# Kernel optimization log

Measured on AMD Instinct MI355X. Metric: run time of the kernel, lower is better.

The kernel has to match this reference:

```python
import jax, jax.numpy as jnp
import numpy as np
from functools import partial

EPS = 1e-3  # keras LayerNormalization default epsilon

def _conv_same(inp, w):
    # inp: [B,H,W,Cin], w: [k,k,Cin,Cout]
    return jax.lax.conv_general_dilated(
        inp, w, window_strides=(1, 1), padding='SAME',
        dimension_numbers=('NHWC', 'HWIO', 'NHWC'))

def _hard_sigmoid(x):
    # keras recurrent_activation default for ConvLSTM2D
    return jnp.clip(0.2 * x + 0.5, 0.0, 1.0)

def setup_inputs() -> dict:
    key = jax.random.key(0)
    k1, k2, k3 = jax.random.split(key, 3)
    B, T, H, W, C, F, K = 4, 16, 64, 64, 32, 64, 3
    x = jax.random.normal(k1, (B, T, H, W, C), dtype=jnp.float32)
    gamma = jnp.ones((C,), jnp.float32)
    beta = jnp.zeros((C,), jnp.float32)
    # gate order i, f, c, o stacked along output channels (keras convention)
    Wx = jax.random.normal(k2, (K, K, C, 4 * F), dtype=jnp.float32) * 0.05
    Wh = jax.random.normal(k3, (K, K, F, 4 * F), dtype=jnp.float32) * 0.05
    b = jnp.zeros((4 * F,), jnp.float32)
    return {"x": x, "gamma": gamma, "beta": beta, "Wx": Wx, "Wh": Wh, "b": b}

def reference(x, gamma, beta, Wx, Wh, b):
    B, T, H, W, C = x.shape
    F = Wh.shape[2]
    # LayerNorm over channel axis
    mu = jnp.mean(x, axis=-1, keepdims=True)
    var = jnp.var(x, axis=-1, keepdims=True)
    xn = (x - mu) * jax.lax.rsqrt(var + EPS) * gamma + beta

    # Precompute input-to-gate convs for all timesteps at once (time folded into batch)
    zx = _conv_same(xn.reshape(B * T, H, W, C), Wx) + b  # [B*T,H,W,4F]
    zx = zx.reshape(B, T, H, W, 4 * F).transpose(1, 0, 2, 3, 4)  # [T,B,H,W,4F]

    def step(carry, zxt):
        h, c = carry
        z = zxt + _conv_same(h, Wh)
        zi, zf, zc, zo = jnp.split(z, 4, axis=-1)
        i = _hard_sigmoid(zi)
        f = _hard_sigmoid(zf)
        c = f * c + i * jnp.tanh(zc)
        o = _hard_sigmoid(zo)
        h = o * jnp.tanh(c)
        return (h, c), h

    h0 = jnp.zeros((B, H, W, F), x.dtype)
    c0 = jnp.zeros((B, H, W, F), x.dtype)
    _, hs = jax.lax.scan(step, (h0, c0), zx)  # hs: [T,B,H,W,F]
    y = hs.transpose(1, 0, 2, 3, 4)  # [B,T,H,W,F] (return_sequences=True)

    # MaxPool3D pool_size=(1,2,2), stride = pool_size, VALID padding
    y = jax.lax.reduce_window(
        y, -jnp.inf, jax.lax.max,
        window_dimensions=(1, 1, 2, 2, 1),
        window_strides=(1, 1, 2, 2, 1),
        padding='VALID')
    return y
```

## Files before the change

### kernel.cpp

```cpp
#include <hip/hip_runtime.h>
#include <hip/hip_fp16.h>

typedef _Float16 f16;
typedef _Float16 f16x8 __attribute__((ext_vector_type(8)));
typedef float f32x4 __attribute__((ext_vector_type(4)));
typedef unsigned long long ull;

#define BB 4
#define TT 16
#define HH 64
#define WW 64
#define CC 32
#define FF 64
#define GG 256

__device__ __forceinline__ float hsig(float z) {
    return fminf(fmaxf(0.2f * z + 0.5f, 0.f), 1.f);
}
__device__ __forceinline__ float tanh_fast(float x) {
    return 1.f - 2.f / (__expf(2.f * x) + 1.f);
}

__device__ __forceinline__ void async_copy16(const void* g, void* l) {
    __builtin_amdgcn_global_load_lds(
        (const __attribute__((address_space(1))) unsigned*)g,
        (__attribute__((address_space(3))) unsigned*)l, 16, 0, 0);
}

__global__ void wprep_kernel(const float* __restrict__ wx, const float* __restrict__ wh,
                             f16* __restrict__ wcat) {
    int e = blockIdx.x * 256 + threadIdx.x;
    if (e < 9 * CC * GG) {
        int n = e & 255, k = e >> 8;
        int p = k / 96, r = k % 96;
        wcat[((p * 12 + (r >> 3)) * 256 + n) * 8 + (r & 7)] = (f16)wx[e];
    } else {
        e -= 9 * CC * GG;
        if (e < 9 * FF * GG) {
            int n = e & 255, k = 288 + (e >> 8);
            int p = k / 96, r = k % 96;
            wcat[((p * 12 + (r >> 3)) * 256 + n) * 8 + (r & 7)] = (f16)wh[e];
        }
    }
}

__global__ __launch_bounds__(512, 2)
void fused_kernel(const float* __restrict__ x, const float* __restrict__ gamma,
                  const float* __restrict__ beta, const f16* __restrict__ wcat,
                  const float* __restrict__ bs, f16* __restrict__ halo,
                  float* __restrict__ out, unsigned* __restrict__ flags) {
    __shared__ __align__(16) f16 patches[3 * 7200];
    __shared__ __align__(16) f16 wbuf[2 * 24576];
    __shared__ float sg[CC], sb[CC];

    f16* xpatch = patches;
    int tid = threadIdx.x;
    int tile = blockIdx.x;
    int bb = tile >> 6, ty = (tile >> 3) & 7, tx = tile & 7;
    int lane = tid & 63, w = tid >> 6;
    int wm = w >> 2, nhalf = (w >> 1) & 1, wn = w & 1;
    int quad = lane >> 4, noff = lane & 15;

    if (tid < CC) sg[tid] = gamma[tid];
    else if (tid < 2 * CC) sb[tid - CC] = beta[tid - CC];

    for (int i = tid; i < 2700; i += 512)
        ((f16x8*)patches)[i] = (f16x8){0, 0, 0, 0, 0, 0, 0, 0};

    const char* gw[6];
#pragma unroll
    for (int i = 0; i < 6; i++) {
        int g = w * 6 + i;
        gw[i] = (const char*)wcat + ((size_t)(g >> 2) * 256 + (g & 3) * 64 + lane) * 16;
    }

    int fch = (nhalf << 5) + (wn << 4) + noff;
    float b_i = bs[fch], b_f = bs[64 + fch], b_c = bs[128 + fch], b_o = bs[192 + fch];

    float creg[2][4];
#pragma unroll
    for (int mt = 0; mt < 2; mt++)
#pragma unroll
        for (int r = 0; r < 4; r++) creg[mt][r] = 0.f;

    int mrow[2];
#pragma unroll
    for (int mt = 0; mt < 2; mt++) {
        int m = (wm << 5) + (mt << 4) + noff;
        mrow[mt] = ((m >> 3) * 10 + (m & 7)) * 72 + (quad << 3);
    }
    int rB[4];
#pragma unroll
    for (int cls = 0; cls < 4; cls++) rB[cls] = ((cls << 6) + fch) << 3;

    __syncthreads();

#pragma unroll
    for (int i = 0; i < 6; i++) {
        int g = w * 6 + i;
        async_copy16(gw[i], &wbuf[(g >> 2) * 2048 + (g & 3) * 512]);
    }

    for (int t = 0; t < TT; t++) {
        f16* hp_cur = patches + 7200 + (t & 1) * 7200;
        f16* hp_nxt = patches + 7200 + ((t + 1) & 1) * 7200;
        f16* wrd0 = &wbuf[(t & 1) * 24576];
        f16* wrd1 = &wbuf[((t + 1) & 1) * 24576];

        if (tid < 200) {
            int pix = tid >> 1, part = tid & 1;
            int py = pix / 10, px_ = pix % 10;
            int gy = ty * 8 - 1 + py, gx = tx * 8 - 1 + px_;
            if (gy >= 0 && gy < HH && gx >= 0 && gx < WW) {
                const float* xp = x + ((size_t)(bb * TT + t) * (HH * WW)
                                       + gy * WW + gx) * CC + part * 16;
                float v[16];
                float s = 0.f, s2 = 0.f;
#pragma unroll
                for (int j = 0; j < 4; j++) {
                    float4 t4 = *(const float4*)(xp + j * 4);
                    v[j * 4] = t4.x; v[j * 4 + 1] = t4.y; v[j * 4 + 2] = t4.z; v[j * 4 + 3] = t4.w;
                    s += t4.x + t4.y + t4.z + t4.w;
                    s2 += t4.x * t4.x + t4.y * t4.y + t4.z * t4.z + t4.w * t4.w;
                }
                s += __shfl_xor(s, 1);
                s2 += __shfl_xor(s2, 1);
                float mu = s * (1.f / CC);
                float var = s2 * (1.f / CC) - mu * mu;
                float rs = rsqrtf(var + 1e-3f);
                f16 o16[16];
#pragma unroll
                for (int c = 0; c < 16; c++)
                    o16[c] = (f16)((v[c] - mu) * rs * sg[part * 16 + c] + sb[part * 16 + c]);
                f16x8* d = (f16x8*)&xpatch[pix * 72 + part * 16];
                d[0] = *(f16x8*)&o16[0];
                d[1] = *(f16x8*)&o16[8];
            }
        }

        f32x4 acc[2][4];
#pragma unroll
        for (int i = 0; i < 2; i++)
#pragma unroll
            for (int j = 0; j < 4; j++) acc[i][j] = (f32x4){0.f, 0.f, 0.f, 0.f};

#pragma unroll
        for (int p = 0; p < 9; ++p) {
            __syncthreads();
            {
                int nc = (p == 8) ? 0 : p + 1;
                f16* wdst = (p & 1) ? wrd0 : wrd1;
#pragma unroll
                for (int i = 0; i < 6; i++) {
                    int g = w * 6 + i;
                    async_copy16(gw[i] + (size_t)nc * 49152,
                                 &wdst[(g >> 2) * 2048 + (g & 3) * 512]);
                }
            }
            const f16* wbp = (p & 1) ? wrd1 : wrd0;
#pragma unroll
            for (int cw = 0; cw < 3; ++cw) {
                int c = p * 3 + cw;
                bool isx = c < 9;
                int hc = c - 9;
                int tap = isx ? c : (hc >> 1);
                int coff = isx ? 0 : ((hc & 1) << 5);
                const f16* ap = isx ? xpatch : hp_cur;
                int dy = tap / 3, dx = tap % 3;
                int toff = (dy * 10 + dx) * 72 + coff;
                f16x8 a[2];
#pragma unroll
                for (int mt = 0; mt < 2; mt++)
                    a[mt] = *(const f16x8*)&ap[mrow[mt] + toff];
#pragma unroll
                for (int cls = 0; cls < 4; cls++) {
                    f16x8 bf = *(const f16x8*)&wbp[((cw << 2) + quad) * 2048 + rB[cls]];
                    acc[0][cls] = __builtin_amdgcn_mfma_f32_16x16x32_f16(a[0], bf, acc[0][cls], 0, 0, 0);
                    acc[1][cls] = __builtin_amdgcn_mfma_f32_16x16x32_f16(a[1], bf, acc[1][cls], 0, 0, 0);
                }
            }
            if (p == 2 && t > 0 && tid >= 256 && tid < 400) {
                int e = tid - 256;
                int hx = e >> 2, quarter = e & 3;
                int py, px_;
                if (hx < 10)      { py = 0; px_ = hx; }
                else if (hx < 20) { py = 9; px_ = hx - 10; }
                else if (hx < 28) { py = 1 + (hx - 20); px_ = 0; }
                else              { py = 1 + (hx - 28); px_ = 9; }
                int gy = ty * 8 - 1 + py, gx = tx * 8 - 1 + px_;
                if (gy >= 0 && gy < HH && gx >= 0 && gx < WW) {
                    int nb = bb * 64 + ((gy >> 3) << 3) + (gx >> 3);
                    while (__hip_atomic_load(&flags[nb], __ATOMIC_RELAXED,
                                             __HIP_MEMORY_SCOPE_AGENT) < (unsigned)t)
                        __builtin_amdgcn_s_sleep(1);
                    const ull* src = (const ull*)(halo + ((size_t)(t * BB + bb) * (HH * WW)
                                                         + gy * WW + gx) * FF) + quarter * 4;
                    f16* dst = &hp_cur[(py * 10 + px_) * 72 + quarter * 16];
#pragma unroll
                    for (int j = 0; j < 4; j++) {
                        ull vv = __hip_atomic_load(src + j, __ATOMIC_RELAXED,
                                                   __HIP_MEMORY_SCOPE_AGENT);
                        *(ull*)(dst + j * 4) = vv;
                    }
                }
            }
        }

#pragma unroll
        for (int mt = 0; mt < 2; mt++) {
#pragma unroll
            for (int r = 0; r < 4; r++) {
                int m = (wm << 5) + (mt << 4) + (quad << 2) + r;
                int py8 = m >> 3, px8 = m & 7;
                float zi = acc[mt][0][r] + b_i;
                float zf = acc[mt][1][r] + b_f;
                float zc = acc[mt][2][r] + b_c;
                float zo = acc[mt][3][r] + b_o;
                float ig = hsig(zi), fg = hsig(zf), og = hsig(zo);
                float cn = fg * creg[mt][r] + ig * tanh_fast(zc);
                creg[mt][r] = cn;
                f16 hval = (f16)(og * tanh_fast(cn));
                hp_nxt[((py8 + 1) * 10 + px8 + 1) * 72 + fch] = hval;
                if (py8 == 0 || py8 == 7 || px8 == 0 || px8 == 7) {
                    union { f16 f; unsigned short u; } cvt; cvt.f = hval;
                    unsigned short* hp = (unsigned short*)halo
                        + ((size_t)((t + 1) * BB + bb) * (HH * WW)
                           + (ty * 8 + py8) * WW + (tx * 8 + px8)) * FF + fch;
                    __hip_atomic_store(hp, cvt.u, __ATOMIC_RELAXED, __HIP_MEMORY_SCOPE_AGENT);
                }
            }
        }
        __syncthreads();
        if (tid == 0)
            __hip_atomic_store(&flags[tile], (unsigned)(t + 1), __ATOMIC_RELAXED,
                               __HIP_MEMORY_SCOPE_AGENT);

        {
            int o = tid * 2;
            int f0 = o & 63;
            int ox2 = (o >> 6) & 3, oy2 = (o >> 8) & 3;
            int row = 1 + oy2 * 2, col = 1 + ox2 * 2;
            const f16* hb = &hp_nxt[(row * 10 + col) * 72 + f0];
            float v0 = fmaxf(fmaxf((float)hb[0], (float)hb[72]),
                             fmaxf((float)hb[720], (float)hb[792]));
            float v1 = fmaxf(fmaxf((float)hb[1], (float)hb[73]),
                             fmaxf((float)hb[721], (float)hb[793]));
            size_t ofs = (((size_t)(bb * TT + t) * 32 + (ty * 4 + oy2)) * 32
                          + (tx * 4 + ox2)) * 64 + f0;
            float2 v2; v2.x = v0; v2.y = v1;
            *(float2*)(out + ofs) = v2;
        }
    }
}

extern "C" void kernel_launch(void* const* d_in, const int* in_sizes, int n_in,
                              void* d_out, int out_size, void* d_ws, size_t ws_size,
                              hipStream_t stream) {
    const float* x = (const float*)d_in[0];
    const float* gamma = (const float*)d_in[1];
    const float* beta = (const float*)d_in[2];
    const float* wx = (const float*)d_in[3];
    const float* wh = (const float*)d_in[4];
    const float* bs = (const float*)d_in[5];
    float* out = (float*)d_out;

    char* ws = (char*)d_ws;
    f16* wcat = (f16*)(ws + 16777216);
    unsigned* flags = (unsigned*)(ws + 17219584);
    f16* hs = (f16*)(ws + 21413888);

    hipMemsetAsync(flags, 0, 256 * 4, stream);
    wprep_kernel<<<864, 256, 0, stream>>>(wx, wh, wcat);

    fused_kernel<<<256, 512, 0, stream>>>(x, gamma, beta, wcat, bs, hs, out, flags);
}
```

Baseline: 265.2 us.

## Pipeline weight chunks through six-slot ring with fine-grained vmcnt waits

Replaces the two-phase double-buffered weight staging (nine phases of three chunks) with a six-slot ring of single-chunk buffers. Each chunk now gets an explicit s_waitcnt vmcnt so MFMAs on early chunks can start before later chunks arrive. Barriers become lgkmcnt-plus-s_barrier. The LayerNorm staging of x for the next timestep and the first weight prefetch are moved to the end of the previous step so they overlap the epilogue. The cost is relying on hand-counted vmcnt values, which can break if the compiler emits extra global loads such as the halo atomics and x loads, and which may serialize the schedule through sched_barrier.

```diff
diff --git a/kernel.cpp b/kernel.cpp
--- a/kernel.cpp
+++ b/kernel.cpp
@@ -13,6 +13,12 @@
 #define CC 32
 #define FF 64
 #define GG 256
+
+#define WAITV(n) do { asm volatile("s_waitcnt vmcnt(" #n ")" ::: "memory"); \
+                      __builtin_amdgcn_sched_barrier(0); } while (0)
+#define LGKBAR do { asm volatile("s_waitcnt lgkmcnt(0)" ::: "memory"); \
+                    __builtin_amdgcn_s_barrier(); \
+                    __builtin_amdgcn_sched_barrier(0); } while (0)
 
 __device__ __forceinline__ float hsig(float z) {
     return fminf(fmaxf(0.2f * z + 0.5f, 0.f), 1.f);
@@ -44,13 +50,49 @@
     }
 }
 
+__device__ __forceinline__ void stage_x(const float* __restrict__ x, int bb, int t,
+                                        int ty, int tx, int tid,
+                                        const float* sg, const float* sb,
+                                        f16* __restrict__ xpatch) {
+    if (tid < 200) {
+        int pix = tid >> 1, part = tid & 1;
+        int py = pix / 10, px_ = pix % 10;
+        int gy = ty * 8 - 1 + py, gx = tx * 8 - 1 + px_;
+        if (gy >= 0 && gy < HH && gx >= 0 && gx < WW) {
+            const float* xp = x + ((size_t)(bb * TT + t) * (HH * WW)
+                                   + gy * WW + gx) * CC + part * 16;
+            float v[16];
+            float s = 0.f, s2 = 0.f;
+#pragma unroll
+            for (int j = 0; j < 4; j++) {
+                float4 t4 = *(const float4*)(xp + j * 4);
+                v[j * 4] = t4.x; v[j * 4 + 1] = t4.y; v[j * 4 + 2] = t4.z; v[j * 4 + 3] = t4.w;
+                s += t4.x + t4.y + t4.z + t4.w;
+                s2 += t4.x * t4.x + t4.y * t4.y + t4.z * t4.z + t4.w * t4.w;
+            }
+            s += __shfl_xor(s, 1);
+            s2 += __shfl_xor(s2, 1);
+            float mu = s * (1.f / CC);
+            float var = s2 * (1.f / CC) - mu * mu;
+            float rs = rsqrtf(var + 1e-3f);
+            f16 o16[16];
+#pragma unroll
+            for (int c = 0; c < 16; c++)
+                o16[c] = (f16)((v[c] - mu) * rs * sg[part * 16 + c] + sb[part * 16 + c]);
+            f16x8* d = (f16x8*)&xpatch[pix * 72 + part * 16];
+            d[0] = *(f16x8*)&o16[0];
+            d[1] = *(f16x8*)&o16[8];
+        }
+    }
+}
+
 __global__ __launch_bounds__(512, 2)
 void fused_kernel(const float* __restrict__ x, const float* __restrict__ gamma,
                   const float* __restrict__ beta, const f16* __restrict__ wcat,
                   const float* __restrict__ bs, f16* __restrict__ halo,
                   float* __restrict__ out, unsigned* __restrict__ flags) {
     __shared__ __align__(16) f16 patches[3 * 7200];
-    __shared__ __align__(16) f16 wbuf[2 * 24576];
+    __shared__ __align__(16) f16 wbuf[6 * 8192];
     __shared__ float sg[CC], sb[CC];
 
     f16* xpatch = patches;
@@ -67,12 +109,7 @@
     for (int i = tid; i < 2700; i += 512)
         ((f16x8*)patches)[i] = (f16x8){0, 0, 0, 0, 0, 0, 0, 0};
 
-    const char* gw[6];
-#pragma unroll
-    for (int i = 0; i < 6; i++) {
-        int g = w * 6 + i;
-        gw[i] = (const char*)wcat + ((size_t)(g >> 2) * 256 + (g & 3) * 64 + lane) * 16;
-    }
+    const char* gwb = (const char*)wcat + w * 2048 + lane * 16;
 
     int fch = (nhalf << 5) + (wn << 4) + noff;
     float b_i = bs[fch], b_f = bs[64 + fch], b_c = bs[128 + fch], b_o = bs[192 + fch];
@@ -95,48 +132,18 @@
 
     __syncthreads();
 
-#pragma unroll
-    for (int i = 0; i < 6; i++) {
-        int g = w * 6 + i;
-        async_copy16(gw[i], &wbuf[(g >> 2) * 2048 + (g & 3) * 512]);
+    stage_x(x, bb, 0, ty, tx, tid, sg, sb, xpatch);
+#pragma unroll
+    for (int k = 0; k < 3; k++) {
+        async_copy16(gwb + (size_t)k * 16384, &wbuf[k * 8192 + w * 1024]);
+        async_copy16(gwb + (size_t)k * 16384 + 1024, &wbuf[k * 8192 + w * 1024 + 512]);
     }
 
     for (int t = 0; t < TT; t++) {
         f16* hp_cur = patches + 7200 + (t & 1) * 7200;
         f16* hp_nxt = patches + 7200 + ((t + 1) & 1) * 7200;
-        f16* wrd0 = &wbuf[(t & 1) * 24576];
-        f16* wrd1 = &wbuf[((t + 1) & 1) * 24576];
-
-        if (tid < 200) {
-            int pix = tid >> 1, part = tid & 1;
-            int py = pix / 10, px_ = pix % 10;
-            int gy = ty * 8 - 1 + py, gx = tx * 8 - 1 + px_;
-            if (gy >= 0 && gy < HH && gx >= 0 && gx < WW) {
-                const float* xp = x + ((size_t)(bb * TT + t) * (HH * WW)
-                                       + gy * WW + gx) * CC + part * 16;
-                float v[16];
-                float s = 0.f, s2 = 0.f;
-#pragma unroll
-                for (int j = 0; j < 4; j++) {
-                    float4 t4 = *(const float4*)(xp + j * 4);
-                    v[j * 4] = t4.x; v[j * 4 + 1] = t4.y; v[j * 4 + 2] = t4.z; v[j * 4 + 3] = t4.w;
-                    s += t4.x + t4.y + t4.z + t4.w;
-                    s2 += t4.x * t4.x + t4.y * t4.y + t4.z * t4.z + t4.w * t4.w;
-                }
-                s += __shfl_xor(s, 1);
-                s2 += __shfl_xor(s2, 1);
-                float mu = s * (1.f / CC);
-                float var = s2 * (1.f / CC) - mu * mu;
-                float rs = rsqrtf(var + 1e-3f);
-                f16 o16[16];
-#pragma unroll
-                for (int c = 0; c < 16; c++)
-                    o16[c] = (f16)((v[c] - mu) * rs * sg[part * 16 + c] + sb[part * 16 + c]);
-                f16x8* d = (f16x8*)&xpatch[pix * 72 + part * 16];
-                d[0] = *(f16x8*)&o16[0];
-                d[1] = *(f16x8*)&o16[8];
-            }
-        }
+
+        LGKBAR;
 
         f32x4 acc[2][4];
 #pragma unroll
@@ -145,41 +152,9 @@
             for (int j = 0; j < 4; j++) acc[i][j] = (f32x4){0.f, 0.f, 0.f, 0.f};
 
 #pragma unroll
-        for (int p = 0; p < 9; ++p) {
-            __syncthreads();
-            {
-                int nc = (p == 8) ? 0 : p + 1;
-                f16* wdst = (p & 1) ? wrd0 : wrd1;
-#pragma unroll
-                for (int i = 0; i < 6; i++) {
-                    int g = w * 6 + i;
-                    async_copy16(gw[i] + (size_t)nc * 49152,
-                                 &wdst[(g >> 2) * 2048 + (g & 3) * 512]);
-                }
-            }
-            const f16* wbp = (p & 1) ? wrd1 : wrd0;
-#pragma unroll
-            for (int cw = 0; cw < 3; ++cw) {
-                int c = p * 3 + cw;
-                bool isx = c < 9;
-                int hc = c - 9;
-                int tap = isx ? c : (hc >> 1);
-                int coff = isx ? 0 : ((hc & 1) << 5);
-                const f16* ap = isx ? xpatch : hp_cur;
-                int dy = tap / 3, dx = tap % 3;
-                int toff = (dy * 10 + dx) * 72 + coff;
-                f16x8 a[2];
-#pragma unroll
-                for (int mt = 0; mt < 2; mt++)
-                    a[mt] = *(const f16x8*)&ap[mrow[mt] + toff];
-#pragma unroll
-                for (int cls = 0; cls < 4; cls++) {
-                    f16x8 bf = *(const f16x8*)&wbp[((cw << 2) + quad) * 2048 + rB[cls]];
-                    acc[0][cls] = __builtin_amdgcn_mfma_f32_16x16x32_f16(a[0], bf, acc[0][cls], 0, 0, 0);
-                    acc[1][cls] = __builtin_amdgcn_mfma_f32_16x16x32_f16(a[1], bf, acc[1][cls], 0, 0, 0);
-                }
-            }
-            if (p == 2 && t > 0 && tid >= 256 && tid < 400) {
+        for (int g = 0; g < 9; ++g) {
+            if (g > 0) LGKBAR;
+            if (g == 2 && t > 0 && tid >= 256 && tid < 400) {
                 int e = tid - 256;
                 int hx = e >> 2, quarter = e & 3;
                 int py, px_;
@@ -202,6 +177,40 @@
                                                    __HIP_MEMORY_SCOPE_AGENT);
                         *(ull*)(dst + j * 4) = vv;
                     }
+                }
+            }
+            if (g < 8) {
+#pragma unroll
+                for (int k = 0; k < 3; k++) {
+                    int c = 3 * g + 3 + k;
+                    async_copy16(gwb + (size_t)c * 16384,
+                                 &wbuf[(c % 6) * 8192 + w * 1024]);
+                    async_copy16(gwb + (size_t)c * 16384 + 1024,
+                                 &wbuf[(c % 6) * 8192 + w * 1024 + 512]);
+                }
+            }
+#pragma unroll
+            for (int cw = 0; cw < 3; ++cw) {
+                int c = g * 3 + cw;
+                if (g < 8) { if (cw == 0) WAITV(10); else if (cw == 1) WAITV(8); else WAITV(6); }
+                else       { if (cw == 0) WAITV(4);  else if (cw == 1) WAITV(2); else WAITV(0); }
+                bool isx = c < 9;
+                int hc = c - 9;
+                int tap = isx ? c : (hc >> 1);
+                int coff = isx ? 0 : ((hc & 1) << 5);
+                const f16* ap = isx ? xpatch : hp_cur;
+                int dy = tap / 3, dx = tap % 3;
+                int toff = (dy * 10 + dx) * 72 + coff;
+                f16x8 a[2];
+#pragma unroll
+                for (int mt = 0; mt < 2; mt++)
+                    a[mt] = *(const f16x8*)&ap[mrow[mt] + toff];
+                const f16* wbc = &wbuf[(c % 6) * 8192 + quad * 2048];
+#pragma unroll
+                for (int cls = 0; cls < 4; cls++) {
+                    f16x8 bf = *(const f16x8*)&wbc[rB[cls]];
+                    acc[0][cls] = __builtin_amdgcn_mfma_f32_16x16x32_f16(a[0], bf, acc[0][cls], 0, 0, 0);
+                    acc[1][cls] = __builtin_amdgcn_mfma_f32_16x16x32_f16(a[1], bf, acc[1][cls], 0, 0, 0);
                 }
             }
         }
@@ -250,6 +259,15 @@
             float2 v2; v2.x = v0; v2.y = v1;
             *(float2*)(out + ofs) = v2;
         }
+
+        if (t + 1 < TT) {
+            stage_x(x, bb, t + 1, ty, tx, tid, sg, sb, xpatch);
+#pragma unroll
+            for (int k = 0; k < 3; k++) {
+                async_copy16(gwb + (size_t)k * 16384, &wbuf[k * 8192 + w * 1024]);
+                async_copy16(gwb + (size_t)k * 16384 + 1024, &wbuf[k * 8192 + w * 1024 + 512]);
+            }
+        }
     }
 }
 
```

Result: faster. 243.1 us (-8.3%).
